# Kernel optimization log

Hardware: AMD Instinct MI355X
Metric: run time of the kernel (lower is better)

Reference implementation:

```python
import jax, jax.numpy as jnp
import numpy as np


def setup_inputs() -> dict:
    key = jax.random.key(0)
    kq, kk, kv = jax.random.split(key, 3)
    B, HQ, HKV, S, D = 1, 32, 8, 2048, 128
    return {
        "query": jax.random.normal(kq, (B, HQ, S, D), dtype=jnp.float32),
        "key": jax.random.normal(kk, (B, HKV, S, D), dtype=jnp.float32),
        "value": jax.random.normal(kv, (B, HKV, S, D), dtype=jnp.float32),
    }


def reference(query, key, value):
    # RawSDP.forward with is_causal=True, attn_mask=None, dropout_p=0, scale=None
    b, hq, sq, d = query.shape
    hkv = key.shape[1]
    reps = hq // hkv  # GQA group size
    # repeak_kv: expand each kv head `reps` times contiguously along head axis
    key = jnp.repeat(key, reps, axis=1)    # [b, hq, skv, d]
    value = jnp.repeat(value, reps, axis=1)
    skv = key.shape[2]
    half_sqrt = 1.0 / jnp.sqrt(jnp.sqrt(jnp.float32(d)))  # scale split across q and k
    scores = jnp.einsum("bhqd,bhkd->bhqk", query * half_sqrt, key * half_sqrt)
    # causal tril bool mask -> additive mask (0 where allowed, finfo.min where not)
    causal = jnp.tril(jnp.ones((sq, skv), dtype=bool))
    neg = jnp.finfo(query.dtype).min
    scores = scores + jnp.where(causal, jnp.zeros((), query.dtype), neg)
    # softmax computed in float32, cast back to query dtype
    attn = jax.nn.softmax(scores.astype(jnp.float32), axis=-1).astype(query.dtype)
    return jnp.einsum("bhqk,bhkd->bhqd", attn, value)
```

## Files before the change

### kernel.cpp

```cpp
#include <hip/hip_runtime.h>
#include <hip/hip_bf16.h>
#include <stdint.h>

typedef __attribute__((ext_vector_type(8))) short bf16x8;
typedef __attribute__((ext_vector_type(4))) float f32x4;
typedef __attribute__((ext_vector_type(16))) float f32x16;

#define S_LEN 2048
#define D_DIM 128
#define HQ_N  32
#define NT32  64
#define SUB_B 8192

__device__ __forceinline__ ushort f2bf(float f) {
  union { float f; uint32_t u; } c; c.f = f;
  uint32_t u = c.u;
  u += 0x7FFFu + ((u >> 16) & 1u);
  return (ushort)(u >> 16);
}

__device__ __forceinline__ uint32_t cvtpk(float lo, float hi) {
  uint32_t r;
  asm("v_cvt_pk_bf16_f32 %0, %1, %2" : "=v"(r) : "v"(lo), "v"(hi));
  return r;
}

__device__ __forceinline__ float xhalf_max(float x) {
  uint32_t a = __builtin_bit_cast(uint32_t, x), b;
  asm volatile("v_mov_b32 %0, %1" : "=&v"(b) : "v"(a));
  asm volatile("v_permlane32_swap_b32 %0, %1" : "+v"(a), "+v"(b));
  return fmaxf(__builtin_bit_cast(float, a), __builtin_bit_cast(float, b));
}

__global__ __launch_bounds__(256) void prep_k(const float* __restrict__ K,
                                              ushort* __restrict__ KT) {
  int tid  = blockIdx.x * 256 + threadIdx.x;
  int tile = tid >> 9;
  int c    = tid & 511;
  int s    = c >> 6;
  int lane = c & 63;
  int l31  = lane & 31, hi = lane >> 5;
  const float* src = K + ((size_t)(tile * 32 + l31)) * D_DIM + 16 * s + 8 * hi;
  float4 x = *(const float4*)src;
  float4 y = *(const float4*)(src + 4);
  union { ushort u[8]; bf16x8 v; } o;
  o.u[0] = f2bf(x.x); o.u[1] = f2bf(x.y); o.u[2] = f2bf(x.z); o.u[3] = f2bf(x.w);
  o.u[4] = f2bf(y.x); o.u[5] = f2bf(y.y); o.u[6] = f2bf(y.z); o.u[7] = f2bf(y.w);
  *(bf16x8*)(KT + (size_t)tid * 8) = o.v;
}

__global__ __launch_bounds__(256) void prep_v(const float* __restrict__ V,
                                              ushort* __restrict__ VT) {
  int tid  = blockIdx.x * 256 + threadIdx.x;
  int tile = tid >> 9;
  int cc   = tid & 511;
  int l31  = cc & 31;
  int hi   = (cc >> 5) & 1;
  int c    = (cc >> 6) & 1;
  int dt   = cc >> 7;
  int hkv  = tile >> 6, ktv = tile & 63;
  const float* src = V + ((size_t)hkv * S_LEN + ktv * 32 + 16 * c + 8 * hi) * D_DIM
                       + 32 * dt + l31;
  union { ushort u[8]; bf16x8 v; } o;
  #pragma unroll
  for (int jj = 0; jj < 8; ++jj) o.u[jj] = f2bf(src[(size_t)jj * D_DIM]);
  *(bf16x8*)(VT + (size_t)tid * 8) = o.v;
}

__device__ __forceinline__ void step_pipe(
    int kt, int j, int qrow, int hi, int lane,
    const char* kt_base, const char* vt_base,
    const bf16x8 (&qf)[8],
    bf16x8 (&KC)[8], bf16x8 (&VC)[8],
    bf16x8 (&KN)[8], bf16x8 (&VN)[8],
    const bf16x8& ones, const f32x16& zero16,
    f32x16 (&o4)[4], float& mrow, float& lsum) {
  if (kt < j) {
    const char* kp2 = kt_base + (size_t)(kt + 1) * SUB_B;
    #pragma unroll
    for (int s = 0; s < 8; ++s)
      KN[s] = *(const bf16x8*)(kp2 + (s * 64 + lane) * 16);
  }
  __builtin_amdgcn_sched_barrier(0);

  f32x16 st = {};
  __builtin_amdgcn_s_setprio(1);
  #pragma unroll
  for (int s = 0; s < 8; ++s)
    st = __builtin_amdgcn_mfma_f32_32x32x16_bf16(KC[s], qf[s], st, 0, 0, 0);
  __builtin_amdgcn_s_setprio(0);
  __builtin_amdgcn_sched_barrier(0);

  if (kt < j) {
    const char* vp2 = vt_base + (size_t)(kt + 1) * SUB_B;
    #pragma unroll
    for (int u = 0; u < 8; ++u)
      VN[u] = *(const bf16x8*)(vp2 + (u * 64 + lane) * 16);
  }
  __builtin_amdgcn_sched_barrier(0);

  if (kt == j) {
    #pragma unroll
    for (int r = 0; r < 16; ++r) {
      int kv = 32 * kt + (r & 3) + 8 * (r >> 2) + 4 * hi;
      if (kv > qrow) st[r] = -1e30f;
    }
  }

  float t8[8];
  #pragma unroll
  for (int e = 0; e < 8; ++e) t8[e] = fmaxf(st[e], st[e + 8]);
  float mx = fmaxf(fmaxf(fmaxf(t8[0], t8[1]), fmaxf(t8[2], t8[3])),
                   fmaxf(fmaxf(t8[4], t8[5]), fmaxf(t8[6], t8[7])));
  mx = xhalf_max(mx);
  if (!__all(mx <= mrow + 8.0f)) {
    float mnew = fmaxf(mrow, mx);
    float alpha = exp2f(mrow - mnew);
    #pragma unroll
    for (int dt = 0; dt < 4; ++dt) o4[dt] *= alpha;
    lsum *= alpha;
    mrow = mnew;
  }
  #pragma unroll
  for (int e = 0; e < 16; ++e) st[e] = exp2f(st[e] - mrow);

  bf16x8 pb[2];
  #pragma unroll
  for (int c = 0; c < 2; ++c) {
    const int r0 = c * 8;
    uint32_t a0 = cvtpk(st[r0 + 0], st[r0 + 1]);
    uint32_t b0 = cvtpk(st[r0 + 4], st[r0 + 5]);
    asm volatile("v_permlane32_swap_b32 %0, %1" : "+v"(a0), "+v"(b0));
    uint32_t a1 = cvtpk(st[r0 + 2], st[r0 + 3]);
    uint32_t b1 = cvtpk(st[r0 + 6], st[r0 + 7]);
    asm volatile("v_permlane32_swap_b32 %0, %1" : "+v"(a1), "+v"(b1));
    union { uint32_t u[4]; bf16x8 v; } pu;
    pu.u[0] = a0; pu.u[1] = a1; pu.u[2] = b0; pu.u[3] = b1;
    pb[c] = pu.v;
  }

  f32x16 pbsum = __builtin_amdgcn_mfma_f32_32x32x16_bf16(ones, pb[0], zero16, 0, 0, 0);
  pbsum = __builtin_amdgcn_mfma_f32_32x32x16_bf16(ones, pb[1], pbsum, 0, 0, 0);
  __builtin_amdgcn_s_setprio(1);
  #pragma unroll
  for (int dt = 0; dt < 4; ++dt) {
    o4[dt] = __builtin_amdgcn_mfma_f32_32x32x16_bf16(VC[2 * dt + 0], pb[0], o4[dt], 0, 0, 0);
    o4[dt] = __builtin_amdgcn_mfma_f32_32x32x16_bf16(VC[2 * dt + 1], pb[1], o4[dt], 0, 0, 0);
  }
  __builtin_amdgcn_s_setprio(0);
  lsum += pbsum[0];
}

__global__ __launch_bounds__(64, 2) void attn_fwd(
    const float* __restrict__ Q, const ushort* __restrict__ KT,
    const ushort* __restrict__ VT, float* __restrict__ O) {
  const int id   = blockIdx.x;
  const int g    = id & 7;
  const int c    = (id >> 3) & 31;
  const int qh   = (id >> 8) & 3;
  const int p    = (id >> 10) & 1;
  const int j    = p ? (63 - c) : c;
  const int h    = g * 4 + qh;
  const int lane = threadIdx.x;
  const int l31  = lane & 31;
  const int hi   = lane >> 5;
  const int qrow = j * 32 + l31;

  const char* kt_base = (const char*)KT + (size_t)g * NT32 * SUB_B;
  const char* vt_base = (const char*)VT + (size_t)g * NT32 * SUB_B;

  const float scale = 0.08838834764831845f * 1.4426950408889634f;
  bf16x8 qf[8];
  {
    const float* qp = Q + ((size_t)h * S_LEN + qrow) * D_DIM;
    #pragma unroll
    for (int s = 0; s < 8; ++s) {
      const float* px = qp + 16 * s + 8 * hi;
      float4 x = *(const float4*)px;
      float4 y = *(const float4*)(px + 4);
      bf16x8 f;
      f[0] = (short)f2bf(x.x * scale); f[1] = (short)f2bf(x.y * scale);
      f[2] = (short)f2bf(x.z * scale); f[3] = (short)f2bf(x.w * scale);
      f[4] = (short)f2bf(y.x * scale); f[5] = (short)f2bf(y.y * scale);
      f[6] = (short)f2bf(y.z * scale); f[7] = (short)f2bf(y.w * scale);
      qf[s] = f;
    }
  }

  bf16x8 ones;
  #pragma unroll
  for (int s = 0; s < 8; ++s) ones[s] = (short)0x3F80;
  const f32x16 zero16 = {};

  f32x16 o4[4] = {};
  float mrow = -1e30f, lsum = 0.f;

  bf16x8 KA[8], VA[8], KB[8], VB[8];
  #pragma unroll
  for (int s = 0; s < 8; ++s)
    KA[s] = *(const bf16x8*)(kt_base + (s * 64 + lane) * 16);
  #pragma unroll
  for (int u = 0; u < 8; ++u)
    VA[u] = *(const bf16x8*)(vt_base + (u * 64 + lane) * 16);

  int kt = 0;
  for (;;) {
    step_pipe(kt, j, qrow, hi, lane, kt_base, vt_base, qf, KA, VA, KB, VB,
              ones, zero16, o4, mrow, lsum);
    if (++kt > j) break;
    step_pipe(kt, j, qrow, hi, lane, kt_base, vt_base, qf, KB, VB, KA, VA,
              ones, zero16, o4, mrow, lsum);
    if (++kt > j) break;
  }

  const float inv = 1.0f / lsum;
  float* op = O + ((size_t)h * S_LEN + qrow) * D_DIM;
  #pragma unroll
  for (int dt = 0; dt < 4; ++dt)
    #pragma unroll
    for (int rq = 0; rq < 4; ++rq) {
      f32x4 vv;
      #pragma unroll
      for (int jj = 0; jj < 4; ++jj) vv[jj] = o4[dt][rq * 4 + jj] * inv;
      *(f32x4*)(op + 32 * dt + 8 * rq + 4 * hi) = vv;
    }
}

extern "C" void kernel_launch(void* const* d_in, const int* in_sizes, int n_in,
                              void* d_out, int out_size, void* d_ws, size_t ws_size,
                              hipStream_t stream) {
  const float* Q = (const float*)d_in[0];
  const float* K = (const float*)d_in[1];
  const float* V = (const float*)d_in[2];
  float* O = (float*)d_out;
  ushort* wsK = (ushort*)d_ws;
  ushort* wsV = wsK + (size_t)8 * NT32 * (SUB_B / 2);
  prep_k<<<1024, 256, 0, stream>>>(K, wsK);
  prep_v<<<1024, 256, 0, stream>>>(V, wsV);
  attn_fwd<<<2048, 64, 0, stream>>>(Q, wsK, wsV, O);
}
```

Before: 89.32 us.

## Split causal attention KV range into chunks with a separate combine kernel

Replaces the single attention kernel with a split-KV scheme. Each query tile's causal KV range is cut into chunks of up to 16 tiles, giving 5120 units with balanced work. Each unit writes bf16 partial outputs plus its row max and sum to workspace, and a new combine kernel merges them with log-sum-exp weighting. The aim is to fix load imbalance and raise occupancy. The cost is an extra launch and partial-output traffic, bf16 rounding of the partials, and the loss of the double-buffered K/V prefetch, since loads are now issued inline.

```diff
diff --git a/kernel.cpp b/kernel.cpp
--- a/kernel.cpp
+++ b/kernel.cpp
@@ -11,6 +11,10 @@
 #define HQ_N  32
 #define NT32  64
 #define SUB_B 8192
+#define UNITS_PER_HEAD 160
+#define N_UNITS 5120
+#define PO_OFF  (8u * 1024 * 1024)
+#define ML_OFF  (PO_OFF + (size_t)N_UNITS * 8192)
 
 __device__ __forceinline__ ushort f2bf(float f) {
   union { float f; uint32_t u; } c; c.f = f;
@@ -30,6 +34,13 @@
   asm volatile("v_mov_b32 %0, %1" : "=&v"(b) : "v"(a));
   asm volatile("v_permlane32_swap_b32 %0, %1" : "+v"(a), "+v"(b));
   return fmaxf(__builtin_bit_cast(float, a), __builtin_bit_cast(float, b));
+}
+
+__device__ __forceinline__ int pfx(int j) {
+  if (j < 16) return j;
+  if (j < 32) return 16 + 2 * (j - 16);
+  if (j < 48) return 48 + 3 * (j - 32);
+  return 96 + 4 * (j - 48);
 }
 
 __global__ __launch_bounds__(256) void prep_k(const float* __restrict__ K,
@@ -67,100 +78,23 @@
   *(bf16x8*)(VT + (size_t)tid * 8) = o.v;
 }
 
-__device__ __forceinline__ void step_pipe(
-    int kt, int j, int qrow, int hi, int lane,
-    const char* kt_base, const char* vt_base,
-    const bf16x8 (&qf)[8],
-    bf16x8 (&KC)[8], bf16x8 (&VC)[8],
-    bf16x8 (&KN)[8], bf16x8 (&VN)[8],
-    const bf16x8& ones, const f32x16& zero16,
-    f32x16 (&o4)[4], float& mrow, float& lsum) {
-  if (kt < j) {
-    const char* kp2 = kt_base + (size_t)(kt + 1) * SUB_B;
-    #pragma unroll
-    for (int s = 0; s < 8; ++s)
-      KN[s] = *(const bf16x8*)(kp2 + (s * 64 + lane) * 16);
-  }
-  __builtin_amdgcn_sched_barrier(0);
-
-  f32x16 st = {};
-  __builtin_amdgcn_s_setprio(1);
-  #pragma unroll
-  for (int s = 0; s < 8; ++s)
-    st = __builtin_amdgcn_mfma_f32_32x32x16_bf16(KC[s], qf[s], st, 0, 0, 0);
-  __builtin_amdgcn_s_setprio(0);
-  __builtin_amdgcn_sched_barrier(0);
-
-  if (kt < j) {
-    const char* vp2 = vt_base + (size_t)(kt + 1) * SUB_B;
-    #pragma unroll
-    for (int u = 0; u < 8; ++u)
-      VN[u] = *(const bf16x8*)(vp2 + (u * 64 + lane) * 16);
-  }
-  __builtin_amdgcn_sched_barrier(0);
-
-  if (kt == j) {
-    #pragma unroll
-    for (int r = 0; r < 16; ++r) {
-      int kv = 32 * kt + (r & 3) + 8 * (r >> 2) + 4 * hi;
-      if (kv > qrow) st[r] = -1e30f;
-    }
-  }
-
-  float t8[8];
-  #pragma unroll
-  for (int e = 0; e < 8; ++e) t8[e] = fmaxf(st[e], st[e + 8]);
-  float mx = fmaxf(fmaxf(fmaxf(t8[0], t8[1]), fmaxf(t8[2], t8[3])),
-                   fmaxf(fmaxf(t8[4], t8[5]), fmaxf(t8[6], t8[7])));
-  mx = xhalf_max(mx);
-  if (!__all(mx <= mrow + 8.0f)) {
-    float mnew = fmaxf(mrow, mx);
-    float alpha = exp2f(mrow - mnew);
-    #pragma unroll
-    for (int dt = 0; dt < 4; ++dt) o4[dt] *= alpha;
-    lsum *= alpha;
-    mrow = mnew;
-  }
-  #pragma unroll
-  for (int e = 0; e < 16; ++e) st[e] = exp2f(st[e] - mrow);
-
-  bf16x8 pb[2];
-  #pragma unroll
-  for (int c = 0; c < 2; ++c) {
-    const int r0 = c * 8;
-    uint32_t a0 = cvtpk(st[r0 + 0], st[r0 + 1]);
-    uint32_t b0 = cvtpk(st[r0 + 4], st[r0 + 5]);
-    asm volatile("v_permlane32_swap_b32 %0, %1" : "+v"(a0), "+v"(b0));
-    uint32_t a1 = cvtpk(st[r0 + 2], st[r0 + 3]);
-    uint32_t b1 = cvtpk(st[r0 + 6], st[r0 + 7]);
-    asm volatile("v_permlane32_swap_b32 %0, %1" : "+v"(a1), "+v"(b1));
-    union { uint32_t u[4]; bf16x8 v; } pu;
-    pu.u[0] = a0; pu.u[1] = a1; pu.u[2] = b0; pu.u[3] = b1;
-    pb[c] = pu.v;
-  }
-
-  f32x16 pbsum = __builtin_amdgcn_mfma_f32_32x32x16_bf16(ones, pb[0], zero16, 0, 0, 0);
-  pbsum = __builtin_amdgcn_mfma_f32_32x32x16_bf16(ones, pb[1], pbsum, 0, 0, 0);
-  __builtin_amdgcn_s_setprio(1);
-  #pragma unroll
-  for (int dt = 0; dt < 4; ++dt) {
-    o4[dt] = __builtin_amdgcn_mfma_f32_32x32x16_bf16(VC[2 * dt + 0], pb[0], o4[dt], 0, 0, 0);
-    o4[dt] = __builtin_amdgcn_mfma_f32_32x32x16_bf16(VC[2 * dt + 1], pb[1], o4[dt], 0, 0, 0);
-  }
-  __builtin_amdgcn_s_setprio(0);
-  lsum += pbsum[0];
-}
-
-__global__ __launch_bounds__(64, 2) void attn_fwd(
+__global__ __launch_bounds__(64, 4) void attn_part(
     const float* __restrict__ Q, const ushort* __restrict__ KT,
-    const ushort* __restrict__ VT, float* __restrict__ O) {
-  const int id   = blockIdx.x;
-  const int g    = id & 7;
-  const int c    = (id >> 3) & 31;
-  const int qh   = (id >> 8) & 3;
-  const int p    = (id >> 10) & 1;
-  const int j    = p ? (63 - c) : c;
-  const int h    = g * 4 + qh;
+    const ushort* __restrict__ VT, char* __restrict__ PO,
+    float* __restrict__ ML) {
+  const int id = blockIdx.x;
+  const int g  = id & 7;
+  const int qh = (id >> 3) & 3;
+  const int h  = g * 4 + qh;
+  const int v  = 159 - (id >> 5);
+  int j, ch;
+  if (v < 16)      { j = v;              ch = 0; }
+  else if (v < 48) { int w = v - 16; j = 16 + (w >> 1); ch = w & 1; }
+  else if (v < 96) { int w = v - 48; int q3 = w / 3; j = 32 + q3; ch = w - 3 * q3; }
+  else             { int w = v - 96; j = 48 + (w >> 2); ch = w & 3; }
+  const int kt0 = ch * 16;
+  const int kt1 = min(kt0 + 16, j + 1);
+
   const int lane = threadIdx.x;
   const int l31  = lane & 31;
   const int hi   = lane >> 5;
@@ -195,35 +129,126 @@
   f32x16 o4[4] = {};
   float mrow = -1e30f, lsum = 0.f;
 
-  bf16x8 KA[8], VA[8], KB[8], VB[8];
-  #pragma unroll
-  for (int s = 0; s < 8; ++s)
-    KA[s] = *(const bf16x8*)(kt_base + (s * 64 + lane) * 16);
-  #pragma unroll
-  for (int u = 0; u < 8; ++u)
-    VA[u] = *(const bf16x8*)(vt_base + (u * 64 + lane) * 16);
-
-  int kt = 0;
-  for (;;) {
-    step_pipe(kt, j, qrow, hi, lane, kt_base, vt_base, qf, KA, VA, KB, VB,
-              ones, zero16, o4, mrow, lsum);
-    if (++kt > j) break;
-    step_pipe(kt, j, qrow, hi, lane, kt_base, vt_base, qf, KB, VB, KA, VA,
-              ones, zero16, o4, mrow, lsum);
-    if (++kt > j) break;
-  }
-
-  const float inv = 1.0f / lsum;
-  float* op = O + ((size_t)h * S_LEN + qrow) * D_DIM;
+  for (int kt = kt0; kt < kt1; ++kt) {
+    const char* kp = kt_base + (size_t)kt * SUB_B;
+    const char* vp = vt_base + (size_t)kt * SUB_B;
+
+    bf16x8 kf[8], vf[8];
+    #pragma unroll
+    for (int s = 0; s < 8; ++s)
+      kf[s] = *(const bf16x8*)(kp + (s * 64 + lane) * 16);
+    #pragma unroll
+    for (int u = 0; u < 8; ++u)
+      vf[u] = *(const bf16x8*)(vp + (u * 64 + lane) * 16);
+
+    f32x16 st = {};
+    __builtin_amdgcn_s_setprio(1);
+    #pragma unroll
+    for (int s = 0; s < 8; ++s)
+      st = __builtin_amdgcn_mfma_f32_32x32x16_bf16(kf[s], qf[s], st, 0, 0, 0);
+    __builtin_amdgcn_s_setprio(0);
+
+    if (kt == j) {
+      #pragma unroll
+      for (int r = 0; r < 16; ++r) {
+        int kv = 32 * kt + (r & 3) + 8 * (r >> 2) + 4 * hi;
+        if (kv > qrow) st[r] = -1e30f;
+      }
+    }
+
+    float t8[8];
+    #pragma unroll
+    for (int e = 0; e < 8; ++e) t8[e] = fmaxf(st[e], st[e + 8]);
+    float mx = fmaxf(fmaxf(fmaxf(t8[0], t8[1]), fmaxf(t8[2], t8[3])),
+                     fmaxf(fmaxf(t8[4], t8[5]), fmaxf(t8[6], t8[7])));
+    mx = xhalf_max(mx);
+    if (!__all(mx <= mrow + 8.0f)) {
+      float mnew = fmaxf(mrow, mx);
+      float alpha = exp2f(mrow - mnew);
+      #pragma unroll
+      for (int dt = 0; dt < 4; ++dt) o4[dt] *= alpha;
+      lsum *= alpha;
+      mrow = mnew;
+    }
+    #pragma unroll
+    for (int e = 0; e < 16; ++e) st[e] = exp2f(st[e] - mrow);
+
+    bf16x8 pb[2];
+    #pragma unroll
+    for (int c = 0; c < 2; ++c) {
+      const int r0 = c * 8;
+      uint32_t a0 = cvtpk(st[r0 + 0], st[r0 + 1]);
+      uint32_t b0 = cvtpk(st[r0 + 4], st[r0 + 5]);
+      asm volatile("v_permlane32_swap_b32 %0, %1" : "+v"(a0), "+v"(b0));
+      uint32_t a1 = cvtpk(st[r0 + 2], st[r0 + 3]);
+      uint32_t b1 = cvtpk(st[r0 + 6], st[r0 + 7]);
+      asm volatile("v_permlane32_swap_b32 %0, %1" : "+v"(a1), "+v"(b1));
+      union { uint32_t u[4]; bf16x8 v; } pu;
+      pu.u[0] = a0; pu.u[1] = a1; pu.u[2] = b0; pu.u[3] = b1;
+      pb[c] = pu.v;
+    }
+
+    f32x16 pbsum = __builtin_amdgcn_mfma_f32_32x32x16_bf16(ones, pb[0], zero16, 0, 0, 0);
+    pbsum = __builtin_amdgcn_mfma_f32_32x32x16_bf16(ones, pb[1], pbsum, 0, 0, 0);
+    __builtin_amdgcn_s_setprio(1);
+    #pragma unroll
+    for (int dt = 0; dt < 4; ++dt) {
+      o4[dt] = __builtin_amdgcn_mfma_f32_32x32x16_bf16(vf[2 * dt + 0], pb[0], o4[dt], 0, 0, 0);
+      o4[dt] = __builtin_amdgcn_mfma_f32_32x32x16_bf16(vf[2 * dt + 1], pb[1], o4[dt], 0, 0, 0);
+    }
+    __builtin_amdgcn_s_setprio(0);
+    lsum += pbsum[0];
+  }
+
+  const int slot = h * UNITS_PER_HEAD + pfx(j) + ch;
+  char* po = PO + (size_t)slot * 8192 + l31 * 256;
   #pragma unroll
   for (int dt = 0; dt < 4; ++dt)
     #pragma unroll
     for (int rq = 0; rq < 4; ++rq) {
-      f32x4 vv;
-      #pragma unroll
-      for (int jj = 0; jj < 4; ++jj) vv[jj] = o4[dt][rq * 4 + jj] * inv;
-      *(f32x4*)(op + 32 * dt + 8 * rq + 4 * hi) = vv;
-    }
+      uint32_t u0 = cvtpk(o4[dt][rq * 4 + 0], o4[dt][rq * 4 + 1]);
+      uint32_t u1 = cvtpk(o4[dt][rq * 4 + 2], o4[dt][rq * 4 + 3]);
+      uint2 uu = {u0, u1};
+      *(uint2*)(po + (32 * dt + 8 * rq + 4 * hi) * 2) = uu;
+    }
+  if (hi == 0) {
+    float2 mlv = {mrow, lsum};
+    *(float2*)(ML + (size_t)slot * 64 + l31 * 2) = mlv;
+  }
+}
+
+__global__ __launch_bounds__(128) void comb(const char* __restrict__ PO,
+                                            const float* __restrict__ ML,
+                                            float* __restrict__ O) {
+  const int b = blockIdx.x;
+  const int h = b >> 6, j = b & 63;
+  const int k = 1 + (j >> 4);
+  const int base = h * UNITS_PER_HEAD + pfx(j);
+  const int d = threadIdx.x;
+
+  __shared__ float sm[4][32][2];
+  if (threadIdx.x < 32) {
+    for (int c = 0; c < k; ++c) {
+      float2 v = *(const float2*)(ML + (size_t)(base + c) * 64 + threadIdx.x * 2);
+      sm[c][threadIdx.x][0] = v.x;
+      sm[c][threadIdx.x][1] = v.y;
+    }
+  }
+  __syncthreads();
+
+  for (int q = 0; q < 32; ++q) {
+    float M = -1e30f;
+    for (int c = 0; c < k; ++c) M = fmaxf(M, sm[c][q][0]);
+    float L = 0.f, acc = 0.f;
+    for (int c = 0; c < k; ++c) {
+      float wgt = exp2f(sm[c][q][0] - M);
+      L += sm[c][q][1] * wgt;
+      ushort pv = *(const ushort*)(PO + (size_t)(base + c) * 8192 + q * 256 + d * 2);
+      uint32_t fu = ((uint32_t)pv) << 16;
+      acc += wgt * __builtin_bit_cast(float, fu);
+    }
+    O[((size_t)h * S_LEN + j * 32 + q) * D_DIM + d] = acc / L;
+  }
 }
 
 extern "C" void kernel_launch(void* const* d_in, const int* in_sizes, int n_in,
@@ -235,7 +260,10 @@
   float* O = (float*)d_out;
   ushort* wsK = (ushort*)d_ws;
   ushort* wsV = wsK + (size_t)8 * NT32 * (SUB_B / 2);
+  char*   PO  = (char*)d_ws + PO_OFF;
+  float*  ML  = (float*)((char*)d_ws + ML_OFF);
   prep_k<<<1024, 256, 0, stream>>>(K, wsK);
   prep_v<<<1024, 256, 0, stream>>>(V, wsV);
-  attn_fwd<<<2048, 64, 0, stream>>>(Q, wsK, wsV, O);
-}
+  attn_part<<<N_UNITS, 64, 0, stream>>>(Q, wsK, wsV, PO, ML);
+  comb<<<HQ_N * 64, 128, 0, stream>>>(PO, ML, O);
+}
```

Result: slower. 306.2 us (+242.9%).
